# Kernel tuning notes

Measured on AMD Instinct MI355X. Metric: run time of the kernel, lower is better.

## Reference

```python
import jax, jax.numpy as jnp
from jax import lax
import numpy as np

V = 400_000   # total vertices (hits)
K = 64        # neighbours per vertex
NSEG = 4      # events (row-split segments)
SEG = V // NSEG


def setup_inputs() -> dict:
    key = jax.random.key(0)
    k1, k2 = jax.random.split(key)
    # neighbour indices constrained to each vertex's own row-split segment
    base = (jnp.arange(V, dtype=jnp.int32) // SEG) * SEG
    neighs = base[:, None] + jax.random.randint(k1, (V, K), 0, SEG, dtype=jnp.int32)
    neighs = neighs.at[:, 0].set(jnp.arange(V, dtype=jnp.int32))  # self as first neighbour (KNN convention)
    hier = jax.random.normal(k2, (V, 1), dtype=jnp.float32)
    row_splits = jnp.arange(NSEG + 1, dtype=jnp.int32) * SEG
    return {"neighs": neighs, "hier": hier, "row_splits": row_splits}


def _local_cluster(neighs, hier, row_splits):
    Vn = neighs.shape[0]
    vidx = jnp.arange(Vn, dtype=jnp.int32)
    # per-segment descending argsort of hier (== the raw_call per-row-split argsort loop)
    seg_id = (jnp.searchsorted(row_splits, vidx, side='right') - 1).astype(jnp.int32)
    order = jnp.lexsort((-hier[:, 0], seg_id)).astype(jnp.int32)  # primary: seg, secondary: hier desc
    order = lax.stop_gradient(order)

    def body(i, st):
        assigned, cluster_of, sel, n_sel = st
        v = order[i]
        is_new = jnp.logical_not(assigned[v])      # v not yet absorbed -> becomes a new centre
        cid = n_sel
        nb = neighs[v]                              # (K,)
        nb_ok = nb >= 0
        nbc = jnp.where(nb_ok, nb, v)               # safe index for padded (-1) neighbours
        take = is_new & nb_ok & jnp.logical_not(assigned[nbc])
        cluster_of = cluster_of.at[nbc].set(jnp.where(take, cid, cluster_of[nbc]))
        assigned = assigned.at[nbc].set(assigned[nbc] | take)
        # the centre itself always belongs to its own cluster
        cluster_of = cluster_of.at[v].set(jnp.where(is_new, cid, cluster_of[v]))
        assigned = assigned.at[v].set(True)
        sel = sel.at[cid].set(jnp.where(is_new, v, sel[cid]))
        n_sel = n_sel + is_new.astype(jnp.int32)
        return (assigned, cluster_of, sel, n_sel)

    init = (jnp.zeros(Vn, bool),
            jnp.zeros(Vn, jnp.int32),
            jnp.full((Vn,), -1, jnp.int32),   # sel padded with -1 (true length = n_sel)
            jnp.int32(0))
    assigned, cluster_of, sel, n_sel = lax.fori_loop(0, Vn, body, init)

    # new row splits: number of centres before each original boundary
    valid = sel >= 0
    is_center = (jnp.zeros(Vn, jnp.int32).at[jnp.where(valid, sel, 0)]
                 .add(valid.astype(jnp.int32))) > 0
    counts = jnp.cumsum(is_center.astype(jnp.int32))
    rs = jnp.concatenate([jnp.zeros(1, jnp.int32), counts[row_splits[1:] - 1]])
    return sel.reshape(-1, 1), rs, cluster_of.reshape(-1, 1)


_local_cluster_jit = jax.jit(_local_cluster)


def reference(neighs, hier, row_splits):
    # returns (sel [V,1] padded with -1, new row_splits [nseg+1], ggather [V,1])
    return _local_cluster_jit(neighs, hier, row_splits)
```

## Files before the change

### kernel.cpp

```cpp
#include <hip/hip_runtime.h>
#include <stdint.h>

typedef unsigned long long ull;

static __device__ __forceinline__ ull packkey(float f, int v) {
    uint32_t u = __float_as_uint(f);
    u = (u & 0x80000000u) ? ~u : (u | 0x80000000u);
    return ((ull)u << 32) | (ull)(~(uint32_t)v);
}
static __device__ __forceinline__ unsigned aloadu32(const unsigned* p) {
    return __hip_atomic_load(p, __ATOMIC_RELAXED, __HIP_MEMORY_SCOPE_AGENT);
}

__global__ void k_build4(const int* __restrict__ neighs, const float* __restrict__ hier,
                         unsigned* __restrict__ word, long E4, int K) {
    long t = (long)blockIdx.x * blockDim.x + threadIdx.x;
    if (t >= E4) return;
    long e = t * 4;
    int u = (int)(e / K);
    ull ku = packkey(hier[u], u);
    int4 w4 = *(const int4*)(neighs + e);
    int ws[4] = {w4.x, w4.y, w4.z, w4.w};
    #pragma unroll
    for (int j = 0; j < 4; j++) {
        int w = ws[j];
        if (w < 0) continue;
        if (ku > packkey(hier[w], w))
            atomicAdd(&word[w], 0x10000u);
    }
}
__global__ void k_build1(const int* __restrict__ neighs, const float* __restrict__ hier,
                         unsigned* __restrict__ word, long E, int K) {
    long e = (long)blockIdx.x * blockDim.x + threadIdx.x;
    if (e >= E) return;
    int w = neighs[e];
    if (w < 0) return;
    int u = (int)(e / K);
    if (packkey(hier[u], u) > packkey(hier[w], w))
        atomicAdd(&word[w], 0x10000u);
}

static __device__ __forceinline__ bool sweep_group(
    int gb, bool pend, int lane,
    const int* __restrict__ neighs, const float* __restrict__ hier,
    unsigned* __restrict__ word, int K, bool& found)
{
    if (!__any(pend)) return pend;
    int v = gb + lane;
    unsigned wd = 0x7FFF0000u;
    if (pend) wd = aloadu32(&word[v]);
    bool absn = pend && ((wd & 0xFFFFu) != 0u);
    bool cenn = pend && (wd == 0u);
    bool dec = absn || cenn;
    ull mdec = __ballot(dec);
    if (!mdec) return pend;
    found = true;
    ull mcen = __ballot(cenn);

    while (mdec) {
        int ls[4];
        int nb = 0;
        while (nb < 4 && mdec) {
            int l = __ffsll((unsigned long long)mdec) - 1;
            mdec &= mdec - 1;
            ls[nb++] = l;
        }
        #pragma unroll
        for (int j = nb; j < 4; j++) ls[j] = -1;

        int vv[4]; ull kv[4]; unsigned dj[4];
        #pragma unroll
        for (int j = 0; j < 4; j++) {
            vv[j] = 0; kv[j] = 0; dj[j] = 0;
            if (ls[j] >= 0) {
                vv[j] = gb + ls[j];
                dj[j] = ((mcen >> ls[j]) & 1ull) ? 0xFFFF0001u : 0xFFFF0000u;
                kv[j] = packkey(hier[vv[j]], vv[j]);
            }
        }
        for (int k0 = 0; k0 < K; k0 += 64) {
            int k = k0 + lane;
            bool kok = k < K;
            #pragma unroll
            for (int j = 0; j < 4; j++) {
                if (ls[j] >= 0 && kok) {
                    int w = neighs[(size_t)vv[j] * (size_t)K + k];
                    if (w >= 0 && kv[j] > packkey(hier[w], w))
                        atomicAdd(&word[w], dj[j]);
                }
            }
        }
    }
    return pend && !dec;
}

__global__ __launch_bounds__(256, 4)
void k_propagate(const int* __restrict__ neighs, const float* __restrict__ hier,
                 unsigned* __restrict__ word, int V, int K, int nwaves) {
    const int gtid = blockIdx.x * blockDim.x + threadIdx.x;
    const int wv = gtid >> 6, lane = gtid & 63;
    const int G = (V + 63) >> 6;
    int gb0 = (wv < G) ? (wv << 6) : -1;
    int g1 = wv + nwaves;
    int gb1 = (g1 < G) ? (g1 << 6) : -1;
    bool p0 = gb0 >= 0 && gb0 + lane < V;
    bool p1 = gb1 >= 0 && gb1 + lane < V;

    long sweeps = 0;
    while (__any(p0 || p1)) {
        bool found = false;
        p0 = sweep_group(gb0, p0, lane, neighs, hier, word, K, found);
        p1 = sweep_group(gb1, p1, lane, neighs, hier, word, K, found);
        if (found) {
            sweeps = 0;
        } else {
            __builtin_amdgcn_s_sleep(2);
            if (++sweeps > 1000000L) break;
        }
    }
}

__global__ void k_absorb(const int* __restrict__ neighs, const float* __restrict__ hier,
                         const unsigned* __restrict__ word, ull* __restrict__ best,
                         int V, int K, int NW) {
    const int gtid = blockIdx.x * blockDim.x + threadIdx.x;
    const int wv = gtid >> 6, lane = gtid & 63;
    const int G = (V + 63) >> 6;
    for (int g = wv; g < G; g += NW) {
        int v = (g << 6) + lane;
        bool cenv = (v < V) && ((word[v] & 0xFFFFu) == 0u);
        ull cm = __ballot(cenv);
        while (cm) {
            int l = __ffsll((unsigned long long)cm) - 1;
            cm &= cm - 1;
            int u = (g << 6) + l;
            ull ku = packkey(hier[u], u);
            const int* row = neighs + (size_t)u * (size_t)K;
            for (int k0 = 0; k0 < K; k0 += 64) {
                int k = k0 + lane;
                int w = (k < K) ? row[k] : -1;
                if (w >= 0 && ku > packkey(hier[w], w))
                    atomicMax(&best[w], ku);
            }
        }
    }
}

__global__ void k_compact(const float* __restrict__ hier,
                          const unsigned* __restrict__ word,
                          const int* __restrict__ row_splits,
                          ull* __restrict__ segKeys,
                          int* __restrict__ segIds,
                          int* __restrict__ counters,
                          int V, int NSEG) {
    int v = blockIdx.x * blockDim.x + threadIdx.x;
    int lane = threadIdx.x & 63;
    bool isc = (v < V) && ((word[v] & 0xFFFFu) == 0u);
    int s = 0;
    if (isc) { while (s + 1 < NSEG && v >= row_splits[s + 1]) s++; }
    if (!__any(isc)) return;
    for (int s0 = 0; s0 < NSEG; s0++) {
        ull ms = __ballot(isc && s == s0);
        if (!ms) continue;
        int leader = __ffsll((unsigned long long)ms) - 1;
        int n = __popcll(ms);
        unsigned base = 0;
        if (lane == leader) base = (unsigned)atomicAdd(&counters[s0], n);
        base = (unsigned)__shfl((int)base, leader);
        unsigned pre = (unsigned)__popcll(ms & ((1ull << lane) - 1ull));
        if (isc && s == s0) {
            int slot = row_splits[s0] + (int)(base + pre);
            segKeys[slot] = packkey(hier[v], v);
            segIds[slot] = v;
        }
    }
}

__global__ void k_rs(const int* __restrict__ counters,
                     int* __restrict__ rsBase,
                     int* __restrict__ rs_out,
                     int NSEG) {
    if (blockIdx.x == 0 && threadIdx.x == 0) {
        int acc = 0;
        rs_out[0] = 0;
        for (int s = 0; s < NSEG; s++) {
            rsBase[s] = acc;
            acc += counters[s];
            rs_out[s + 1] = acc;
        }
    }
}

#define RTILE 1024
__global__ void k_rank(const ull* __restrict__ segKeys,
                       const int* __restrict__ segIds,
                       const int* __restrict__ counters,
                       const int* __restrict__ rsBase,
                       const int* __restrict__ row_splits,
                       int* __restrict__ cidOf,
                       int* __restrict__ sel_out,
                       int V, int NSEG) {
    __shared__ ull tile[RTILE];
    int t = blockIdx.x * blockDim.x + threadIdx.x;
    int s = 0;
    if (t < V) { while (s + 1 < NSEG && t >= row_splits[s + 1]) s++; }
    int base = (t < V) ? row_splits[s] : 0;
    int j = (t < V) ? (t - base) : -1;
    int cnt = (t < V) ? counters[s] : 0;
    bool active = (t < V) && (j >= 0) && (j < cnt);
    ull mk = active ? segKeys[t] : 0ull;
    int r = 0;

    int B0 = blockIdx.x * blockDim.x;
    int B1 = min(B0 + (int)blockDim.x - 1, V - 1);
    int sf = 0; while (sf + 1 < NSEG && B0 >= row_splits[sf + 1]) sf++;
    int sl = 0; while (sl + 1 < NSEG && B1 >= row_splits[sl + 1]) sl++;

    for (int s0 = sf; s0 <= sl; s0++) {
        int b0 = row_splits[s0];
        int c0 = counters[s0];
        bool in = active && (s == s0);
        for (int tb = 0; tb < c0; tb += RTILE) {
            int n = min(RTILE, c0 - tb);
            __syncthreads();
            for (int i = threadIdx.x; i < n; i += blockDim.x)
                tile[i] = segKeys[b0 + tb + i];
            __syncthreads();
            if (in) {
                int rr = 0;
                #pragma unroll 8
                for (int i = 0; i < n; i++) rr += (tile[i] > mk) ? 1 : 0;
                r += rr;
            }
        }
    }
    if (active) {
        int cid = rsBase[s] + r;
        int v = segIds[t];
        cidOf[v] = cid;
        sel_out[cid] = v;
    }
}

__global__ void k_assign(const ull* __restrict__ best,
                         const int* __restrict__ cidOf,
                         int* __restrict__ clus_out,
                         int V) {
    int v = blockIdx.x * blockDim.x + threadIdx.x;
    if (v >= V) return;
    ull b = best[v];
    int c;
    if (b == 0ull) {
        c = cidOf[v];
    } else {
        uint32_t a = ~(uint32_t)(b & 0xFFFFFFFFull);
        c = cidOf[a];
    }
    clus_out[v] = c;
}

extern "C" void kernel_launch(void* const* d_in, const int* in_sizes, int n_in,
                              void* d_out, int out_size, void* d_ws, size_t ws_size,
                              hipStream_t stream) {
    const int*   neighs     = (const int*)d_in[0];
    const float* hier       = (const float*)d_in[1];
    const int*   row_splits = (const int*)d_in[2];

    const int V    = in_sizes[1];
    const int K    = in_sizes[0] / V;
    const int NSEG = in_sizes[2] - 1;
    const long E   = (long)V * (long)K;

    int* out      = (int*)d_out;
    int* sel_out  = out;
    int* rs_out   = out + V;
    int* clus_out = out + V + NSEG + 1;

    char* w = (char*)d_ws;
    ull*      best    = (ull*)(w);
    unsigned* word    = (unsigned*)(w + (size_t)8 * V);
    int*      cnts    = (int*)(w + (size_t)12 * V);
    int*      rsBase  = (int*)(w + (size_t)12 * V + 128);
    size_t segOff     = (size_t)12 * V + 256;
    ull*      segKeys = (ull*)(w + segOff);
    int*      segIds  = (int*)(w + segOff + (size_t)8 * V);
    int*      cidOf   = (int*)(w + segOff + (size_t)12 * V);

    const int B  = 256;
    const int gV = (V + B - 1) / B;

    (void)hipMemsetAsync(w, 0, segOff, stream);
    (void)hipMemsetAsync(sel_out, 0xFF, (size_t)4 * V, stream);

    if ((K & 3) == 0) {
        long E4 = E / 4;
        k_build4<<<(int)((E4 + B - 1) / B), B, 0, stream>>>(neighs, hier, word, E4, K);
    } else {
        k_build1<<<(int)((E + B - 1) / B), B, 0, stream>>>(neighs, hier, word, E, K);
    }

    const int PB = 1024;
    const int NW = PB * B / 64;
    k_propagate<<<PB, B, 0, stream>>>(neighs, hier, word, V, K, NW);

    k_absorb<<<PB, B, 0, stream>>>(neighs, hier, word, best, V, K, NW);
    k_compact<<<gV, B, 0, stream>>>(hier, word, row_splits, segKeys, segIds, cnts, V, NSEG);
    k_rs<<<1, 64, 0, stream>>>(cnts, rsBase, rs_out, NSEG);
    k_rank<<<gV, B, 0, stream>>>(segKeys, segIds, cnts, rsBase, row_splits,
                                 cidOf, sel_out, V, NSEG);
    k_assign<<<gV, B, 0, stream>>>(best, cidOf, clus_out, V);
}
```

Before: 1.288 ms.

## Fuse absorb pass into propagate and double persistent wave count

The separate k_absorb kernel is removed. Each centre now does an atomicMax of its key into best[w] for lower-priority neighbours while it propagates, which saves a second pass over the neighbour rows of all centres. The persistent propagate grid is doubled (2048 blocks, launch bounds raised to 8 blocks per CU) so each wave handles fewer vertex groups, and the spin timeout is doubled. The cost is extra atomics inside the latency-critical propagation loop and higher register pressure from the raised occupancy target. The persistent spin-waiting scheme also relies on all blocks being resident at once, and more blocks makes that harder to guarantee.

```diff
diff --git a/kernel.cpp b/kernel.cpp
--- a/kernel.cpp
+++ b/kernel.cpp
@@ -43,7 +43,7 @@
 static __device__ __forceinline__ bool sweep_group(
     int gb, bool pend, int lane,
     const int* __restrict__ neighs, const float* __restrict__ hier,
-    unsigned* __restrict__ word, int K, bool& found)
+    unsigned* __restrict__ word, ull* __restrict__ best, int K, bool& found)
 {
     if (!__any(pend)) return pend;
     int v = gb + lane;
@@ -68,13 +68,14 @@
         #pragma unroll
         for (int j = nb; j < 4; j++) ls[j] = -1;
 
-        int vv[4]; ull kv[4]; unsigned dj[4];
+        int vv[4]; ull kv[4]; unsigned dj[4]; bool cj[4];
         #pragma unroll
         for (int j = 0; j < 4; j++) {
-            vv[j] = 0; kv[j] = 0; dj[j] = 0;
+            vv[j] = 0; kv[j] = 0; dj[j] = 0; cj[j] = false;
             if (ls[j] >= 0) {
                 vv[j] = gb + ls[j];
-                dj[j] = ((mcen >> ls[j]) & 1ull) ? 0xFFFF0001u : 0xFFFF0000u;
+                cj[j] = (mcen >> ls[j]) & 1ull;
+                dj[j] = cj[j] ? 0xFFFF0001u : 0xFFFF0000u;
                 kv[j] = packkey(hier[vv[j]], vv[j]);
             }
         }
@@ -85,8 +86,10 @@
             for (int j = 0; j < 4; j++) {
                 if (ls[j] >= 0 && kok) {
                     int w = neighs[(size_t)vv[j] * (size_t)K + k];
-                    if (w >= 0 && kv[j] > packkey(hier[w], w))
+                    if (w >= 0 && kv[j] > packkey(hier[w], w)) {
                         atomicAdd(&word[w], dj[j]);
+                        if (cj[j]) atomicMax(&best[w], kv[j]);
+                    }
                 }
             }
         }
@@ -94,9 +97,10 @@
     return pend && !dec;
 }
 
-__global__ __launch_bounds__(256, 4)
+__global__ __launch_bounds__(256, 8)
 void k_propagate(const int* __restrict__ neighs, const float* __restrict__ hier,
-                 unsigned* __restrict__ word, int V, int K, int nwaves) {
+                 unsigned* __restrict__ word, ull* __restrict__ best,
+                 int V, int K, int nwaves) {
     const int gtid = blockIdx.x * blockDim.x + threadIdx.x;
     const int wv = gtid >> 6, lane = gtid & 63;
     const int G = (V + 63) >> 6;
@@ -109,39 +113,13 @@
     long sweeps = 0;
     while (__any(p0 || p1)) {
         bool found = false;
-        p0 = sweep_group(gb0, p0, lane, neighs, hier, word, K, found);
-        p1 = sweep_group(gb1, p1, lane, neighs, hier, word, K, found);
+        p0 = sweep_group(gb0, p0, lane, neighs, hier, word, best, K, found);
+        p1 = sweep_group(gb1, p1, lane, neighs, hier, word, best, K, found);
         if (found) {
             sweeps = 0;
         } else {
             __builtin_amdgcn_s_sleep(2);
-            if (++sweeps > 1000000L) break;
-        }
-    }
-}
-
-__global__ void k_absorb(const int* __restrict__ neighs, const float* __restrict__ hier,
-                         const unsigned* __restrict__ word, ull* __restrict__ best,
-                         int V, int K, int NW) {
-    const int gtid = blockIdx.x * blockDim.x + threadIdx.x;
-    const int wv = gtid >> 6, lane = gtid & 63;
-    const int G = (V + 63) >> 6;
-    for (int g = wv; g < G; g += NW) {
-        int v = (g << 6) + lane;
-        bool cenv = (v < V) && ((word[v] & 0xFFFFu) == 0u);
-        ull cm = __ballot(cenv);
-        while (cm) {
-            int l = __ffsll((unsigned long long)cm) - 1;
-            cm &= cm - 1;
-            int u = (g << 6) + l;
-            ull ku = packkey(hier[u], u);
-            const int* row = neighs + (size_t)u * (size_t)K;
-            for (int k0 = 0; k0 < K; k0 += 64) {
-                int k = k0 + lane;
-                int w = (k < K) ? row[k] : -1;
-                if (w >= 0 && ku > packkey(hier[w], w))
-                    atomicMax(&best[w], ku);
-            }
+            if (++sweeps > 2000000L) break;
         }
     }
 }
@@ -299,11 +277,10 @@
         k_build1<<<(int)((E + B - 1) / B), B, 0, stream>>>(neighs, hier, word, E, K);
     }
 
-    const int PB = 1024;
+    const int PB = 2048;
     const int NW = PB * B / 64;
-    k_propagate<<<PB, B, 0, stream>>>(neighs, hier, word, V, K, NW);
-
-    k_absorb<<<PB, B, 0, stream>>>(neighs, hier, word, best, V, K, NW);
+    k_propagate<<<PB, B, 0, stream>>>(neighs, hier, word, best, V, K, NW);
+
     k_compact<<<gV, B, 0, stream>>>(hier, word, row_splits, segKeys, segIds, cnts, V, NSEG);
     k_rs<<<1, 64, 0, stream>>>(cnts, rsBase, rs_out, NSEG);
     k_rank<<<gV, B, 0, stream>>>(segKeys, segIds, cnts, rsBase, row_splits,
```

After: 1.284 ms. No clear change (-0.3%).
